# Kernel tuning notes

Measured on AMD Instinct MI355X. Metric: run time of the kernel, lower is better.

The kernel has to match this reference:

```python
import jax, jax.numpy as jnp
import numpy as np

B, T, C = 2, 2048, 1024
N_HEAD = 16
HEAD_DIM = C // N_HEAD
ROPE_BASE = 10000.0


def setup_inputs() -> dict:
    key = jax.random.key(0)
    ks = jax.random.split(key, 5)
    s = 0.02
    return {
        "x": jax.random.normal(ks[0], (B, T, C), dtype=jnp.float32),
        "Wq": jax.random.normal(ks[1], (C, C), dtype=jnp.float32) * s,
        "Wk": jax.random.normal(ks[2], (C, C), dtype=jnp.float32) * s,
        "Wv": jax.random.normal(ks[3], (C, C), dtype=jnp.float32) * s,
        "Wo": jax.random.normal(ks[4], (C, C), dtype=jnp.float32) * s,
    }


def _rope_cos_sin(seq_len, head_dim, dtype):
    inv_freq = 1.0 / (ROPE_BASE ** (jnp.arange(0, head_dim, 2, dtype=jnp.float32) / head_dim))
    t = jnp.arange(seq_len, dtype=jnp.float32)
    freqs = jnp.einsum("i,j->ij", t, inv_freq)          # [T, head_dim/2]
    emb = jnp.concatenate([freqs, freqs], axis=-1)        # [T, head_dim]
    return jnp.cos(emb).astype(dtype), jnp.sin(emb).astype(dtype)


def _rotate_half(x):
    x1, x2 = jnp.split(x, 2, axis=-1)
    return jnp.concatenate([-x2, x1], axis=-1)


def _mha(x, Wq, Wk, Wv, Wo):
    b, t, c = x.shape
    # torch nn.Linear stores weight [out, in]: y = x @ W.T
    q = (x @ Wq.T).reshape(b, t, N_HEAD, HEAD_DIM).transpose(0, 2, 1, 3)  # [B,H,T,D]
    k = (x @ Wk.T).reshape(b, t, N_HEAD, HEAD_DIM).transpose(0, 2, 1, 3)
    v = (x @ Wv.T).reshape(b, t, N_HEAD, HEAD_DIM).transpose(0, 2, 1, 3)
    cos, sin = _rope_cos_sin(t, HEAD_DIM, x.dtype)        # [T,D] each, broadcast over B,H
    q = q * cos + _rotate_half(q) * sin
    k = k * cos + _rotate_half(k) * sin
    scale = 1.0 / np.sqrt(HEAD_DIM).astype(np.float32)
    att = jnp.einsum("bhqd,bhkd->bhqk", q, k) * scale     # [B,H,T,T]
    causal = jnp.tril(jnp.ones((t, t), dtype=bool))
    att = jnp.where(causal, att, jnp.finfo(att.dtype).min)
    att = jax.nn.softmax(att, axis=-1)
    y = jnp.einsum("bhqk,bhkd->bhqd", att, v)             # [B,H,T,D]
    y = y.transpose(0, 2, 1, 3).reshape(b, t, c)
    return y @ Wo.T


def reference(x, Wq, Wk, Wv, Wo):
    return _mha(x, Wq, Wk, Wv, Wo)
```

## Files before the change

kernel.cpp:

```cpp
#include <hip/hip_runtime.h>

#define BB 2
#define TT 2048
#define CC 1024
#define NH 16
#define HD 64

typedef __attribute__((ext_vector_type(8))) short bf16x8;
typedef __attribute__((ext_vector_type(4))) float floatx4;
typedef __attribute__((ext_vector_type(16))) float floatx16;

__device__ __forceinline__ unsigned short f2bf(float f) {
    union { float f; unsigned int u; } v; v.f = f;
    unsigned int u = v.u;
    u = (u + 0x7fffu + ((u >> 16) & 1u)) >> 16;
    return (unsigned short)u;
}
__device__ __forceinline__ float bf2f(unsigned short u) {
    return __uint_as_float((unsigned)u << 16);
}

typedef __attribute__((address_space(3))) unsigned char* lds_ptr_t;
typedef const __attribute__((address_space(1))) unsigned char* glob_ptr_t;
__device__ __forceinline__ void gll16(const void* g, void* l) {
    __builtin_amdgcn_global_load_lds((glob_ptr_t)g, (lds_ptr_t)l, 16, 0, 0);
}

__global__ __launch_bounds__(256) void cast_all_k(const float* __restrict__ x,
                                                  const float* __restrict__ wq,
                                                  const float* __restrict__ wk,
                                                  const float* __restrict__ wv,
                                                  const float* __restrict__ wo,
                                                  unsigned short* __restrict__ xb,
                                                  unsigned short* __restrict__ wqkvb,
                                                  unsigned short* __restrict__ wob,
                                                  float2* __restrict__ tabQ,
                                                  float2* __restrict__ tabK) {
    if (blockIdx.x >= 8192) {
        int idx = (blockIdx.x - 8192) * 256 + threadIdx.x;
        int t = idx >> 5, j = idx & 31;
        const float C1 = 0.41524101186092f;
        const float I2PI = 0.15915494309189535f;
        float rev = (float)t * (__builtin_amdgcn_exp2f(-(float)j * C1) * I2PI);
        rev -= floorf(rev);
        float ang = rev * 6.2831853071796f;
        float c = __cosf(ang), s = __sinf(ang);
        const float qs = 0.18033688011112f;
        tabK[idx] = make_float2(c, s);
        tabQ[idx] = make_float2(c * qs, s * qs);
        return;
    }
    int i = blockIdx.x * 256 + threadIdx.x;
    const float* src;
    unsigned short* dst;
    if (i < 1048576) {
        src = x + (size_t)i * 4;
        dst = xb + (size_t)i * 4;
    } else {
        int w   = (i - 1048576) >> 18;
        int off = (i - 1048576) & 262143;
        const float* s0 = (w == 0) ? wq : (w == 1) ? wk : (w == 2) ? wv : wo;
        unsigned short* d0 = (w == 3) ? wob : (wqkvb + (size_t)w * 1048576);
        src = s0 + (size_t)off * 4;
        dst = d0 + (size_t)off * 4;
    }
    float4 v = *(const float4*)src;
    ushort4 o;
    o.x = f2bf(v.x); o.y = f2bf(v.y); o.z = f2bf(v.z); o.w = f2bf(v.w);
    *(ushort4*)dst = o;
}

__global__ __launch_bounds__(256, 2) void gemm_o_k(const unsigned short* __restrict__ A,
                                                   const unsigned short* __restrict__ Bt,
                                                   float* __restrict__ C, int N, int K) {
    __shared__ __align__(16) unsigned short As[128][64];
    __shared__ __align__(16) unsigned short Bs[64][64];
    const int tid  = threadIdx.x;
    const int wave = tid >> 6;
    const int lane = tid & 63;
    const int quad = lane >> 4;
    const int l16  = lane & 15;
    const int sw   = l16 & 7;
    const int wr = (wave >> 1) * 64;
    const int wc = (wave & 1) * 32;
    const int bid = blockIdx.x;
    const int xcd = bid & 7, sl = bid >> 3;
    const int row0 = (xcd * 4 + (sl >> 4)) * 128;
    const int col0 = (sl & 15) * 64;
    const int w8r = wave * 8 + (lane >> 3);
    const int cg  = ((lane & 7) ^ (lane >> 3)) * 8;
    const int cl  = (lane & 7) * 8;

    const unsigned short* Ap = A  + (size_t)(row0 + w8r) * K + cg;
    const unsigned short* Bp = Bt + (size_t)(col0 + w8r) * K + cg;

    floatx4 acc[4][2];
    #pragma unroll
    for (int i = 0; i < 4; i++)
        #pragma unroll
        for (int j = 0; j < 2; j++) acc[i][j] = (floatx4){0.f, 0.f, 0.f, 0.f};

    for (int k0 = 0; k0 < K; k0 += 64) {
        __syncthreads();
        #pragma unroll
        for (int isu = 0; isu < 4; isu++)
            gll16(Ap + (size_t)(isu * 32) * K + k0, &As[isu * 32 + w8r][cl]);
        #pragma unroll
        for (int isu = 0; isu < 2; isu++)
            gll16(Bp + (size_t)(isu * 32) * K + k0, &Bs[isu * 32 + w8r][cl]);
        __syncthreads();
        #pragma unroll
        for (int kk = 0; kk < 2; kk++) {
            bf16x8 af[4], bfr[2];
            #pragma unroll
            for (int i = 0; i < 4; i++)
                af[i]  = *(const bf16x8*)&As[wr + 16 * i + l16][((kk * 4 + quad) ^ sw) * 8];
            #pragma unroll
            for (int j = 0; j < 2; j++)
                bfr[j] = *(const bf16x8*)&Bs[wc + 16 * j + l16][((kk * 4 + quad) ^ sw) * 8];
            #pragma unroll
            for (int i = 0; i < 4; i++)
                #pragma unroll
                for (int j = 0; j < 2; j++)
                    acc[i][j] = __builtin_amdgcn_mfma_f32_16x16x32_bf16(af[i], bfr[j], acc[i][j], 0, 0, 0);
        }
    }

    #pragma unroll
    for (int i = 0; i < 4; i++)
        #pragma unroll
        for (int j = 0; j < 2; j++)
            #pragma unroll
            for (int r = 0; r < 4; r++) {
                int row = row0 + wr + 16 * i + quad * 4 + r;
                int col = col0 + wc + 16 * j + l16;
                C[(size_t)row * N + col] = acc[i][j][r];
            }
}

__global__ __launch_bounds__(256) void gemm_qkv_k(const unsigned short* __restrict__ A,
                                                  const unsigned short* __restrict__ Bt,
                                                  const float2* __restrict__ tabQ,
                                                  const float2* __restrict__ tabK,
                                                  unsigned short* __restrict__ Qb,
                                                  unsigned short* __restrict__ Kb,
                                                  unsigned short* __restrict__ Vb) {
    __shared__ __align__(16) unsigned short SMEM[128 * 128];
    unsigned short (*As)[64] = (unsigned short(*)[64])SMEM;
    unsigned short (*Bs)[64] = (unsigned short(*)[64])(SMEM + 128 * 64);
    unsigned short (*Eb)[128] = (unsigned short(*)[128])SMEM;
    const int K = 1024;
    const int tid  = threadIdx.x;
    const int wave = tid >> 6;
    const int lane = tid & 63;
    const int quad = lane >> 4;
    const int l16  = lane & 15;
    const int sw   = l16 & 7;
    const int wr = (wave >> 1) * 64;
    const int wc = (wave & 1) * 64;
    const int bid = blockIdx.x;
    const int xcd = bid & 7, sl = bid >> 3;
    const int row0 = (xcd * 4 + sl / 24) * 128;
    const int col0 = (sl % 24) * 128;
    const int w8r = wave * 8 + (lane >> 3);
    const int cg  = ((lane & 7) ^ (lane >> 3)) * 8;
    const int cl  = (lane & 7) * 8;

    const unsigned short* Ap = A  + (size_t)(row0 + w8r) * K + cg;
    const unsigned short* Bp = Bt + (size_t)(col0 + w8r) * K + cg;

    floatx4 acc[4][4];
    #pragma unroll
    for (int i = 0; i < 4; i++)
        #pragma unroll
        for (int j = 0; j < 4; j++) acc[i][j] = (floatx4){0.f, 0.f, 0.f, 0.f};

    for (int k0 = 0; k0 < K; k0 += 64) {
        __syncthreads();
        #pragma unroll
        for (int isu = 0; isu < 4; isu++) {
            gll16(Ap + (size_t)(isu * 32) * K + k0, &As[isu * 32 + w8r][cl]);
            gll16(Bp + (size_t)(isu * 32) * K + k0, &Bs[isu * 32 + w8r][cl]);
        }
        __syncthreads();
        #pragma unroll
        for (int kk = 0; kk < 2; kk++) {
            bf16x8 af[4], bfr[4];
            #pragma unroll
            for (int i = 0; i < 4; i++)
                af[i]  = *(const bf16x8*)&As[wr + 16 * i + l16][((kk * 4 + quad) ^ sw) * 8];
            #pragma unroll
            for (int j = 0; j < 4; j++)
                bfr[j] = *(const bf16x8*)&Bs[wc + 16 * j + l16][((kk * 4 + quad) ^ sw) * 8];
            #pragma unroll
            for (int i = 0; i < 4; i++)
                #pragma unroll
                for (int j = 0; j < 4; j++)
                    acc[i][j] = __builtin_amdgcn_mfma_f32_16x16x32_bf16(af[i], bfr[j], acc[i][j], 0, 0, 0);
        }
    }

    __syncthreads();
    #pragma unroll
    for (int i = 0; i < 4; i++)
        #pragma unroll
        for (int j = 0; j < 4; j++)
            #pragma unroll
            for (int r = 0; r < 4; r++) {
                int erow = wr + 16 * i + quad * 4 + r;
                int col  = wc + 16 * j + l16;
                int pcol = (((col >> 3) ^ (erow & 15)) << 3) | (col & 7);
                Eb[erow][pcol] = f2bf(acc[i][j][r]);
            }
    __syncthreads();

    const int row  = tid >> 1;
    const int half = tid & 1;
    const int grow = row0 + row;
    const int t    = grow & (TT - 1);
    const int bb   = grow >> 11;
    const int sect = col0 >> 10;
    const int hh   = ((col0 & 1023) >> 6) + half;
    union { int4 q[8]; unsigned short u[64]; } raw;
    #pragma unroll
    for (int i = 0; i < 8; i++) {
        int pg = (half * 8 + i) ^ (row & 15);
        raw.q[i] = *(const int4*)&Eb[row][pg << 3];
    }
    size_t obase = ((size_t)(bb * NH + hh) * TT + t) * 64;
    if (sect == 2) {
        #pragma unroll
        for (int i = 0; i < 8; i++) *(int4*)(Vb + obase + 8 * i) = raw.q[i];
    } else {
        const float4* tab = (const float4*)((sect ? tabK : tabQ) + (size_t)t * 32);
        unsigned short* dst = sect ? Kb : Qb;
        union { int4 q[8]; unsigned short u[64]; } o;
        #pragma unroll
        for (int i = 0; i < 16; i++) {
            float4 cs = tab[i];
            int j0 = 2 * i, j1 = 2 * i + 1;
            float a0 = bf2f(raw.u[j0]), b0 = bf2f(raw.u[j0 + 32]);
            float a1 = bf2f(raw.u[j1]), b1 = bf2f(raw.u[j1 + 32]);
            o.u[j0]      = f2bf(a0 * cs.x - b0 * cs.y);
            o.u[j0 + 32] = f2bf(b0 * cs.x + a0 * cs.y);
            o.u[j1]      = f2bf(a1 * cs.z - b1 * cs.w);
            o.u[j1 + 32] = f2bf(b1 * cs.z + a1 * cs.w);
        }
        #pragma unroll
        for (int i = 0; i < 8; i++) *(int4*)(dst + obase + 8 * i) = o.q[i];
    }
}

__global__ __launch_bounds__(256) void vtr_k(const unsigned short* __restrict__ Vb,
                                             unsigned short* __restrict__ Vt) {
    __shared__ __align__(16) unsigned short Vsh[64][70];
    const int tid = threadIdx.x;
    const int tt = blockIdx.x;
    const int bh = blockIdx.y;
    const int sr = tid >> 2;
    const int sc = (tid & 3) * 16;
    const unsigned short* src = Vb + ((size_t)bh * TT + tt * 64 + sr) * 64 + sc;
    *(int4*)&Vsh[sr][sc]     = *(const int4*)src;
    *(int4*)&Vsh[sr][sc + 8] = *(const int4*)(src + 8);
    __syncthreads();
    const int dr = tid >> 2;
    const int tc = (tid & 3) * 16;
    unsigned short tv[16];
    #pragma unroll
    for (int i = 0; i < 16; i++) {
        int x = tc + i;
        int key = (x & ~15) + (x & 3) + ((x >> 2) & 1) * 8 + ((x >> 3) & 1) * 4;
        tv[i] = Vsh[key][dr];
    }
    size_t vo = ((size_t)bh * 64 + dr) * TT + tt * 64 + tc;
    *(int4*)(Vt + vo)     = *(int4*)&tv[0];
    *(int4*)(Vt + vo + 8) = *(int4*)&tv[8];
}

__global__ __launch_bounds__(256, 4) void flash_k(const unsigned short* __restrict__ Qb,
                                                  const unsigned short* __restrict__ Kb,
                                                  const unsigned short* __restrict__ Vt,
                                                  unsigned short* __restrict__ Yb) {
    __shared__ __align__(16) unsigned short Ks[64][72];
    __shared__ __align__(16) unsigned short Vs[64][72];
    const int tid  = threadIdx.x;
    const int wave = tid >> 6;
    const int lane = tid & 63;
    const int h    = lane >> 5;
    const int l32  = lane & 31;
    const int qt   = 15 - (blockIdx.x >> 5);
    const int bh   = blockIdx.x & 31;
    const int q0 = qt * 128;
    const int qw = q0 + wave * 32 + l32;
    const int sr = tid >> 2;
    const int sc = (tid & 3) * 16;

    bf16x8 qf[4];
    {
        const unsigned short* qp = Qb + ((size_t)bh * TT + qw) * 64 + h * 8;
        #pragma unroll
        for (int kk = 0; kk < 4; kk++) qf[kk] = *(const bf16x8*)(qp + kk * 16);
    }

    floatx16 accO[2];
    accO[0] = (floatx16)(0.f);
    accO[1] = (floatx16)(0.f);
    float lsum = 0.f;

    const int kt1 = 2 * qt + 2;
    const unsigned short* kbase = Kb + (size_t)bh * TT * 64;
    const unsigned short* vbase = Vt + (size_t)bh * 64 * TT;

    const unsigned short* kp = kbase + (size_t)sr * 64 + sc;
    const unsigned short* vp = vbase + (size_t)sr * TT + sc;
    int4 ka = *(const int4*)kp, kb2 = *(const int4*)(kp + 8);
    int4 va = *(const int4*)vp, vb2 = *(const int4*)(vp + 8);

    for (int kt = 0; kt < kt1; kt++) {
        __syncthreads();
        *(int4*)&Ks[sr][sc]     = ka;
        *(int4*)&Ks[sr][sc + 8] = kb2;
        *(int4*)&Vs[sr][sc]     = va;
        *(int4*)&Vs[sr][sc + 8] = vb2;
        __syncthreads();
        if (kt + 1 < kt1) {
            const unsigned short* kp2 = kbase + ((size_t)((kt + 1) * 64) + sr) * 64 + sc;
            const unsigned short* vp2 = vbase + (size_t)sr * TT + (kt + 1) * 64 + sc;
            ka  = *(const int4*)kp2; kb2 = *(const int4*)(kp2 + 8);
            va  = *(const int4*)vp2; vb2 = *(const int4*)(vp2 + 8);
        }

        const bool diag = (kt >= 2 * qt);
        bf16x8 pfrag[4];

        #pragma unroll
        for (int mb = 0; mb < 2; mb++) {
            floatx16 sacc = (floatx16)(0.f);
            __builtin_amdgcn_s_setprio(1);
            #pragma unroll
            for (int kk = 0; kk < 4; kk++) {
                bf16x8 kf = *(const bf16x8*)&Ks[32 * mb + l32][kk * 16 + h * 8];
                sacc = __builtin_amdgcn_mfma_f32_32x32x16_bf16(kf, qf[kk], sacc, 0, 0, 0);
            }
            __builtin_amdgcn_s_setprio(0);
            float p[16];
            const int kmb = kt * 64 + 32 * mb + 4 * h;
            #pragma unroll
            for (int r = 0; r < 16; r++) {
                float pv = __builtin_amdgcn_exp2f(sacc[r]);
                if (diag) {
                    int ki = kmb + (r & 3) + 8 * (r >> 2);
                    if (ki > qw) pv = 0.f;
                }
                lsum += pv;
                p[r] = pv;
            }
            #pragma unroll
            for (int half = 0; half < 2; half++) {
                union { bf16x8 v; unsigned u[4]; } pk;
                #pragma unroll
                for (int i = 0; i < 4; i++) {
                    unsigned ulo = __float_as_uint(p[half * 8 + 2 * i]);
                    unsigned uhi = __float_as_uint(p[half * 8 + 2 * i + 1]);
                    pk.u[i] = (ulo >> 16) | (uhi & 0xffff0000u);
                }
                pfrag[2 * mb + half] = pk.v;
            }
        }

        __builtin_amdgcn_s_setprio(1);
        #pragma unroll
        for (int mbo = 0; mbo < 2; mbo++) {
            #pragma unroll
            for (int kk = 0; kk < 4; kk++) {
                bf16x8 vf = *(const bf16x8*)&Vs[32 * mbo + l32][kk * 16 + h * 8];
                accO[mbo] = __builtin_amdgcn_mfma_f32_32x32x16_bf16(vf, pfrag[kk], accO[mbo], 0, 0, 0);
            }
        }
        __builtin_amdgcn_s_setprio(0);
    }

    lsum += __shfl_xor(lsum, 32);
    const float inv = 1.0f / lsum;
    const int bb = bh >> 4, hh = bh & 15;
    unsigned short* orow = Yb + ((size_t)(bb * TT + qw)) * CC + hh * 64;
    #pragma unroll
    for (int mbo = 0; mbo < 2; mbo++)
        #pragma unroll
        for (int a = 0; a < 4; a++) {
            ushort4 o4;
            o4.x = f2bf(accO[mbo][4 * a + 0] * inv);
            o4.y = f2bf(accO[mbo][4 * a + 1] * inv);
            o4.z = f2bf(accO[mbo][4 * a + 2] * inv);
            o4.w = f2bf(accO[mbo][4 * a + 3] * inv);
            *(ushort4*)(orow + 32 * mbo + 8 * a + 4 * h) = o4;
        }
}

extern "C" void kernel_launch(void* const* d_in, const int* in_sizes, int n_in,
                              void* d_out, int out_size, void* d_ws, size_t ws_size,
                              hipStream_t stream) {
    (void)in_sizes; (void)n_in; (void)out_size; (void)ws_size;
    const float* x  = (const float*)d_in[0];
    const float* Wq = (const float*)d_in[1];
    const float* Wk = (const float*)d_in[2];
    const float* Wv = (const float*)d_in[3];
    const float* Wo = (const float*)d_in[4];
    float* out = (float*)d_out;
    char* ws = (char*)d_ws;

    unsigned short* xb    = (unsigned short*)(ws + 0);
    unsigned short* wqkvb = (unsigned short*)(ws + (8ull  << 20));
    unsigned short* wob   = (unsigned short*)(ws + (14ull << 20));
    unsigned short* Qb    = (unsigned short*)(ws + (16ull << 20));
    unsigned short* Kb    = (unsigned short*)(ws + (24ull << 20));
    unsigned short* Vb    = (unsigned short*)(ws + (32ull << 20));
    unsigned short* Vt    = (unsigned short*)(ws + (40ull << 20));
    unsigned short* Yb    = (unsigned short*)(ws + (48ull << 20));
    float2* tabQ = (float2*)(ws + (73ull << 20));
    float2* tabK = (float2*)(ws + (73ull << 20) + (512ull << 10));

    cast_all_k<<<8448, 256, 0, stream>>>(x, Wq, Wk, Wv, Wo, xb, wqkvb, wob, tabQ, tabK);
    gemm_qkv_k<<<768, 256, 0, stream>>>(xb, wqkvb, tabQ, tabK, Qb, Kb, Vb);
    vtr_k<<<dim3(32, 32), 256, 0, stream>>>(Vb, Vt);
    flash_k<<<512, 256, 0, stream>>>(Qb, Kb, Vt, Yb);
    gemm_o_k<<<512, 256, 0, stream>>>(Yb, wob, out, 1024, 1024);
}
```

Baseline: 186.8 us.

## Split flash attention KV range across wave pairs and merge partial outputs in LDS

The flash kernel now assigns 64-query tiles to 1024 blocks. Each pair of waves splits the causal key range in half, using double-buffered K/V LDS tiles, so both halves are processed at once. Partial accumulators and row sums from the second wave group are merged through LDS before normalization. This adds parallelism and shortens the per-block serial loop. The cost is extra LDS traffic, an extra reduction step and some idle waves when the split is uneven.

```diff
diff --git a/kernel.cpp b/kernel.cpp
--- a/kernel.cpp
+++ b/kernel.cpp
@@ -281,17 +281,22 @@
                                                   const unsigned short* __restrict__ Kb,
                                                   const unsigned short* __restrict__ Vt,
                                                   unsigned short* __restrict__ Yb) {
-    __shared__ __align__(16) unsigned short Ks[64][72];
-    __shared__ __align__(16) unsigned short Vs[64][72];
+    __shared__ __align__(16) unsigned short Ks[2][64][72];
+    __shared__ __align__(16) unsigned short Vs[2][64][72];
     const int tid  = threadIdx.x;
     const int wave = tid >> 6;
     const int lane = tid & 63;
     const int h    = lane >> 5;
     const int l32  = lane & 31;
-    const int qt   = 15 - (blockIdx.x >> 5);
+    const int g    = wave >> 1;
+    const int s    = wave & 1;
+    const int qj   = 31 - (blockIdx.x >> 5);
     const int bh   = blockIdx.x & 31;
-    const int q0 = qt * 128;
-    const int qw = q0 + wave * 32 + l32;
+    const int q0   = qj * 64;
+    const int qw   = q0 + g * 32 + l32;
+    const int nt   = qj + 1;
+    const int n0   = (nt + 1) >> 1;
+    const int n1   = nt - n0;
     const int sr = tid >> 2;
     const int sc = (tid & 3) * 16;
 
@@ -307,94 +312,140 @@
     accO[1] = (floatx16)(0.f);
     float lsum = 0.f;
 
-    const int kt1 = 2 * qt + 2;
     const unsigned short* kbase = Kb + (size_t)bh * TT * 64;
     const unsigned short* vbase = Vt + (size_t)bh * 64 * TT;
 
-    const unsigned short* kp = kbase + (size_t)sr * 64 + sc;
-    const unsigned short* vp = vbase + (size_t)sr * TT + sc;
-    int4 ka = *(const int4*)kp, kb2 = *(const int4*)(kp + 8);
-    int4 va = *(const int4*)vp, vb2 = *(const int4*)(vp + 8);
-
-    for (int kt = 0; kt < kt1; kt++) {
-        __syncthreads();
-        *(int4*)&Ks[sr][sc]     = ka;
-        *(int4*)&Ks[sr][sc + 8] = kb2;
-        *(int4*)&Vs[sr][sc]     = va;
-        *(int4*)&Vs[sr][sc + 8] = vb2;
-        __syncthreads();
-        if (kt + 1 < kt1) {
-            const unsigned short* kp2 = kbase + ((size_t)((kt + 1) * 64) + sr) * 64 + sc;
-            const unsigned short* vp2 = vbase + (size_t)sr * TT + (kt + 1) * 64 + sc;
-            ka  = *(const int4*)kp2; kb2 = *(const int4*)(kp2 + 8);
-            va  = *(const int4*)vp2; vb2 = *(const int4*)(vp2 + 8);
-        }
-
-        const bool diag = (kt >= 2 * qt);
-        bf16x8 pfrag[4];
-
-        #pragma unroll
-        for (int mb = 0; mb < 2; mb++) {
-            floatx16 sacc = (floatx16)(0.f);
+    int4 ka0, kb0, va0, vb0, ka1, kb1, va1, vb1;
+    {
+        const unsigned short* kp = kbase + (size_t)sr * 64 + sc;
+        const unsigned short* vp = vbase + (size_t)sr * TT + sc;
+        ka0 = *(const int4*)kp; kb0 = *(const int4*)(kp + 8);
+        va0 = *(const int4*)vp; vb0 = *(const int4*)(vp + 8);
+        if (n1 > 0) {
+            const unsigned short* kp1 = kbase + ((size_t)(n0 * 64) + sr) * 64 + sc;
+            const unsigned short* vp1 = vbase + (size_t)sr * TT + n0 * 64 + sc;
+            ka1 = *(const int4*)kp1; kb1 = *(const int4*)(kp1 + 8);
+            va1 = *(const int4*)vp1; vb1 = *(const int4*)(vp1 + 8);
+        }
+    }
+
+    for (int i = 0; i < n0; i++) {
+        __syncthreads();
+        *(int4*)&Ks[0][sr][sc]     = ka0;
+        *(int4*)&Ks[0][sr][sc + 8] = kb0;
+        *(int4*)&Vs[0][sr][sc]     = va0;
+        *(int4*)&Vs[0][sr][sc + 8] = vb0;
+        if (i < n1) {
+            *(int4*)&Ks[1][sr][sc]     = ka1;
+            *(int4*)&Ks[1][sr][sc + 8] = kb1;
+            *(int4*)&Vs[1][sr][sc]     = va1;
+            *(int4*)&Vs[1][sr][sc + 8] = vb1;
+        }
+        __syncthreads();
+        if (i + 1 < n0) {
+            const unsigned short* kp = kbase + ((size_t)((i + 1) * 64) + sr) * 64 + sc;
+            const unsigned short* vp = vbase + (size_t)sr * TT + (i + 1) * 64 + sc;
+            ka0 = *(const int4*)kp; kb0 = *(const int4*)(kp + 8);
+            va0 = *(const int4*)vp; vb0 = *(const int4*)(vp + 8);
+            if (i + 1 < n1) {
+                const unsigned short* kp1 = kbase + ((size_t)((n0 + i + 1) * 64) + sr) * 64 + sc;
+                const unsigned short* vp1 = vbase + (size_t)sr * TT + (n0 + i + 1) * 64 + sc;
+                ka1 = *(const int4*)kp1; kb1 = *(const int4*)(kp1 + 8);
+                va1 = *(const int4*)vp1; vb1 = *(const int4*)(vp1 + 8);
+            }
+        }
+
+        const int kt = (s ? n0 : 0) + i;
+        const bool active = (s == 0) || (i < n1);
+        if (active) {
+            const bool diag = (kt == qj);
+            bf16x8 pfrag[4];
+
+            #pragma unroll
+            for (int mb = 0; mb < 2; mb++) {
+                floatx16 sacc = (floatx16)(0.f);
+                __builtin_amdgcn_s_setprio(1);
+                #pragma unroll
+                for (int kk = 0; kk < 4; kk++) {
+                    bf16x8 kf = *(const bf16x8*)&Ks[s][32 * mb + l32][kk * 16 + h * 8];
+                    sacc = __builtin_amdgcn_mfma_f32_32x32x16_bf16(kf, qf[kk], sacc, 0, 0, 0);
+                }
+                __builtin_amdgcn_s_setprio(0);
+                float p[16];
+                const int kmb = kt * 64 + 32 * mb + 4 * h;
+                #pragma unroll
+                for (int r = 0; r < 16; r++) {
+                    float pv = __builtin_amdgcn_exp2f(sacc[r]);
+                    if (diag) {
+                        int ki = kmb + (r & 3) + 8 * (r >> 2);
+                        if (ki > qw) pv = 0.f;
+                    }
+                    lsum += pv;
+                    p[r] = pv;
+                }
+                #pragma unroll
+                for (int half = 0; half < 2; half++) {
+                    union { bf16x8 v; unsigned u[4]; } pk;
+                    #pragma unroll
+                    for (int i2 = 0; i2 < 4; i2++) {
+                        unsigned ulo = __float_as_uint(p[half * 8 + 2 * i2]);
+                        unsigned uhi = __float_as_uint(p[half * 8 + 2 * i2 + 1]);
+                        pk.u[i2] = (ulo >> 16) | (uhi & 0xffff0000u);
+                    }
+                    pfrag[2 * mb + half] = pk.v;
+                }
+            }
+
             __builtin_amdgcn_s_setprio(1);
             #pragma unroll
-            for (int kk = 0; kk < 4; kk++) {
-                bf16x8 kf = *(const bf16x8*)&Ks[32 * mb + l32][kk * 16 + h * 8];
-                sacc = __builtin_amdgcn_mfma_f32_32x32x16_bf16(kf, qf[kk], sacc, 0, 0, 0);
+            for (int mbo = 0; mbo < 2; mbo++) {
+                #pragma unroll
+                for (int kk = 0; kk < 4; kk++) {
+                    bf16x8 vf = *(const bf16x8*)&Vs[s][32 * mbo + l32][kk * 16 + h * 8];
+                    accO[mbo] = __builtin_amdgcn_mfma_f32_32x32x16_bf16(vf, pfrag[kk], accO[mbo], 0, 0, 0);
+                }
             }
             __builtin_amdgcn_s_setprio(0);
-            float p[16];
-            const int kmb = kt * 64 + 32 * mb + 4 * h;
-            #pragma unroll
-            for (int r = 0; r < 16; r++) {
-                float pv = __builtin_amdgcn_exp2f(sacc[r]);
-                if (diag) {
-                    int ki = kmb + (r & 3) + 8 * (r >> 2);
-                    if (ki > qw) pv = 0.f;
-                }
-                lsum += pv;
-                p[r] = pv;
-            }
-            #pragma unroll
-            for (int half = 0; half < 2; half++) {
-                union { bf16x8 v; unsigned u[4]; } pk;
-                #pragma unroll
-                for (int i = 0; i < 4; i++) {
-                    unsigned ulo = __float_as_uint(p[half * 8 + 2 * i]);
-                    unsigned uhi = __float_as_uint(p[half * 8 + 2 * i + 1]);
-                    pk.u[i] = (ulo >> 16) | (uhi & 0xffff0000u);
-                }
-                pfrag[2 * mb + half] = pk.v;
-            }
-        }
-
-        __builtin_amdgcn_s_setprio(1);
-        #pragma unroll
-        for (int mbo = 0; mbo < 2; mbo++) {
-            #pragma unroll
-            for (int kk = 0; kk < 4; kk++) {
-                bf16x8 vf = *(const bf16x8*)&Vs[32 * mbo + l32][kk * 16 + h * 8];
-                accO[mbo] = __builtin_amdgcn_mfma_f32_32x32x16_bf16(vf, pfrag[kk], accO[mbo], 0, 0, 0);
-            }
-        }
-        __builtin_amdgcn_s_setprio(0);
+        }
     }
 
     lsum += __shfl_xor(lsum, 32);
-    const float inv = 1.0f / lsum;
-    const int bb = bh >> 4, hh = bh & 15;
-    unsigned short* orow = Yb + ((size_t)(bb * TT + qw)) * CC + hh * 64;
-    #pragma unroll
-    for (int mbo = 0; mbo < 2; mbo++)
-        #pragma unroll
-        for (int a = 0; a < 4; a++) {
-            ushort4 o4;
-            o4.x = f2bf(accO[mbo][4 * a + 0] * inv);
-            o4.y = f2bf(accO[mbo][4 * a + 1] * inv);
-            o4.z = f2bf(accO[mbo][4 * a + 2] * inv);
-            o4.w = f2bf(accO[mbo][4 * a + 3] * inv);
-            *(ushort4*)(orow + 32 * mbo + 8 * a + 4 * h) = o4;
-        }
+    __syncthreads();
+    float* Fb = (float*)&Ks[0][0][0];
+    float* Lb = (float*)&Vs[0][0][0];
+    if (s == 1) {
+        float* f = Fb + (size_t)(g * 32 + l32) * 65;
+        #pragma unroll
+        for (int mbo = 0; mbo < 2; mbo++)
+            #pragma unroll
+            for (int a = 0; a < 4; a++) {
+                int d0 = 32 * mbo + 8 * a + 4 * h;
+                f[d0 + 0] = accO[mbo][4 * a + 0];
+                f[d0 + 1] = accO[mbo][4 * a + 1];
+                f[d0 + 2] = accO[mbo][4 * a + 2];
+                f[d0 + 3] = accO[mbo][4 * a + 3];
+            }
+        if (lane < 32) Lb[g * 32 + l32] = lsum;
+    }
+    __syncthreads();
+    if (s == 0) {
+        const float* f = Fb + (size_t)(g * 32 + l32) * 65;
+        const float inv = 1.0f / (lsum + Lb[g * 32 + l32]);
+        const int bb = bh >> 4, hh = bh & 15;
+        unsigned short* orow = Yb + ((size_t)(bb * TT + qw)) * CC + hh * 64;
+        #pragma unroll
+        for (int mbo = 0; mbo < 2; mbo++)
+            #pragma unroll
+            for (int a = 0; a < 4; a++) {
+                int d0 = 32 * mbo + 8 * a + 4 * h;
+                ushort4 o4;
+                o4.x = f2bf((accO[mbo][4 * a + 0] + f[d0 + 0]) * inv);
+                o4.y = f2bf((accO[mbo][4 * a + 1] + f[d0 + 1]) * inv);
+                o4.z = f2bf((accO[mbo][4 * a + 2] + f[d0 + 2]) * inv);
+                o4.w = f2bf((accO[mbo][4 * a + 3] + f[d0 + 3]) * inv);
+                *(ushort4*)(orow + d0) = o4;
+            }
+    }
 }
 
 extern "C" void kernel_launch(void* const* d_in, const int* in_sizes, int n_in,
@@ -423,6 +474,6 @@
     cast_all_k<<<8448, 256, 0, stream>>>(x, Wq, Wk, Wv, Wo, xb, wqkvb, wob, tabQ, tabK);
     gemm_qkv_k<<<768, 256, 0, stream>>>(xb, wqkvb, tabQ, tabK, Qb, Kb, Vb);
     vtr_k<<<dim3(32, 32), 256, 0, stream>>>(Vb, Vt);
-    flash_k<<<512, 256, 0, stream>>>(Qb, Kb, Vt, Yb);
+    flash_k<<<1024, 256, 0, stream>>>(Qb, Kb, Vt, Yb);
     gemm_o_k<<<512, 256, 0, stream>>>(Yb, wob, out, 1024, 1024);
 }
```

New measurement: 174.5 us. 6.6% less time.
